# Performance work log

Hardware: AMD Instinct MI355X
Metric: run time of the kernel (lower is better)

## Reference

```python
import jax, jax.numpy as jnp
import numpy as np

B, N, D = 4, 2048, 512
OUT, H = 512, 8
HD = OUT // H

def setup_inputs() -> dict:
    key = jax.random.key(0)
    ks = jax.random.split(key, 10)
    s = 1.0 / np.sqrt(D)
    x = jax.random.normal(ks[0], (B, N, D), dtype=jnp.float32)
    adj = jax.random.randint(ks[1], (N, N), 0, 2, dtype=jnp.int32)
    Wq = jax.random.uniform(ks[2], (D, OUT), jnp.float32, -s, s)
    bq = jax.random.uniform(ks[3], (OUT,), jnp.float32, -s, s)
    Wk = jax.random.uniform(ks[4], (D, OUT), jnp.float32, -s, s)
    bk = jax.random.uniform(ks[5], (OUT,), jnp.float32, -s, s)
    Wv = jax.random.uniform(ks[6], (D, OUT), jnp.float32, -s, s)
    bv = jax.random.uniform(ks[7], (OUT,), jnp.float32, -s, s)
    so = 1.0 / np.sqrt(OUT)
    Wo = jax.random.uniform(ks[8], (OUT, OUT), jnp.float32, -so, so)
    bo = jax.random.uniform(ks[9], (OUT,), jnp.float32, -so, so)
    return {"x": x, "adj": adj, "Wq": Wq, "bq": bq, "Wk": Wk, "bk": bk,
            "Wv": Wv, "bv": bv, "Wo": Wo, "bo": bo}

def reference(x, adj, Wq, bq, Wk, bk, Wv, bv, Wo, bo):
    scale = HD ** -0.5
    # [B,N,OUT] -> [B,H,N,HD]
    def split_heads(t):
        return t.reshape(B, N, H, HD).transpose(0, 2, 1, 3)
    q = split_heads(x @ Wq + bq)
    k = split_heads(x @ Wk + bk)
    v = split_heads(x @ Wv + bv)
    attn = jnp.einsum('bhnd,bhmd->bhnm', q, k) * scale  # [B,H,N,N]
    mask = (adj == 0)[None, None, :, :]
    attn = jnp.where(mask, jnp.float32(-1e9), attn)
    attn = jax.nn.softmax(attn, axis=-1)
    out = jnp.einsum('bhnm,bhmd->bhnd', attn, v)
    out = out.transpose(0, 2, 1, 3).reshape(B, N, OUT)
    return out @ Wo + bo
```

## Files before the change

kernel.cpp:

```cpp
#include <hip/hip_runtime.h>
#include <math.h>

#define NB   4
#define NN   2048
#define DD   512
#define NOUT 512
#define NH   8
#define HDIM 64

typedef __attribute__((ext_vector_type(4))) short bf16x4;
typedef __attribute__((ext_vector_type(8))) short bf16x8;
typedef __attribute__((ext_vector_type(4))) float f32x4;
#define MFMA32(a, b, c)  __builtin_amdgcn_mfma_f32_16x16x32_bf16(a, b, c, 0, 0, 0)

typedef const __attribute__((address_space(1))) unsigned int* gas_ptr;
typedef __attribute__((address_space(3))) unsigned int* las_ptr;

#define SCALE2 0.18033688f


__device__ inline unsigned short f2bf(float f) {
    unsigned int u = __float_as_uint(f);
    u += 0x7fffu + ((u >> 16) & 1u);
    return (unsigned short)(u >> 16);
}

__device__ inline unsigned int pack_trunc(float lo, float hi) {
    return __builtin_amdgcn_perm(__float_as_uint(hi), __float_as_uint(lo), 0x07060302u);
}

__global__ __launch_bounds__(256) void prep(
    const float* __restrict__ x, unsigned short* __restrict__ xt,
    const float* __restrict__ W0, const float* __restrict__ W1,
    const float* __restrict__ W2, const float* __restrict__ W3,
    unsigned short* __restrict__ Tqkv, unsigned short* __restrict__ To,
    const int* __restrict__ adj, unsigned int* __restrict__ amaskW)
{
    const int blk = blockIdx.x;
    const int t   = threadIdx.x;

    if (blk < 2048) {
        const int i = (blk * 256 + t) * 8;
        const int m = i >> 9, k = i & 511;
        float4 a = *(const float4*)(x + i);
        float4 b = *(const float4*)(x + i + 4);
        ushort4 u0, u1;
        u0.x = f2bf(a.x); u0.y = f2bf(a.y); u0.z = f2bf(a.z); u0.w = f2bf(a.w);
        u1.x = f2bf(b.x); u1.y = f2bf(b.y); u1.z = f2bf(b.z); u1.w = f2bf(b.w);
        unsigned short* dst = xt + ((size_t)(m >> 7) * 65536)
                                 + (k >> 5) * 4096 + (m & 127) * 32 + (k & 31);
        *(ushort4*)dst       = u0;
        *(ushort4*)(dst + 4) = u1;
        return;
    }
    if (blk < 2304) {
        __shared__ float tile[64][65];
        const int idx = blk - 2048;
        const int z = idx >> 6, rem = idx & 63;
        const float* W;
        switch (z) {
            case 0:  W = W0; break;
            case 1:  W = W1; break;
            case 2:  W = W2; break;
            default: W = W3; break;
        }
        unsigned short* T = (z < 3) ? Tqkv : To;
        const int ngbase  = (z < 3) ? z * 512 : 0;
        const int k0 = (rem & 7) * 64, n0 = (rem >> 3) * 64;
        const int r = t >> 6, c = t & 63;
#pragma unroll
        for (int rep = 0; rep < 16; ++rep) {
            const int row = rep * 4 + r;
            tile[row][c] = W[(size_t)(k0 + row) * NOUT + n0 + c];
        }
        __syncthreads();
        const int k  = k0 + c;
        const int ks = k >> 5, kk = k & 31;
#pragma unroll
        for (int rep = 0; rep < 16; ++rep) {
            const int row = rep * 4 + r;
            const int ng  = ngbase + n0 + row;
            T[((size_t)(ng >> 7) * 65536) + ks * 4096 + (ng & 127) * 32 + kk]
                = f2bf(tile[c][row]);
        }
        return;
    }
    {
        const int gid  = (blk - 2304) * 256 + t;
        const int w0   = gid * 4;
        const int qrow = w0 >> 10;
        const int wloc = w0 & 1023;
        const int kb0  = wloc * 2;
        int4 a0 = *(const int4*)(adj + (size_t)qrow * NN + kb0);
        int4 a1 = *(const int4*)(adj + (size_t)qrow * NN + kb0 + 4);
        uint4 m;
        m.x = (a0.x ? 0xFFFFu : 0u) | (a0.y ? 0xFFFF0000u : 0u);
        m.y = (a0.z ? 0xFFFFu : 0u) | (a0.w ? 0xFFFF0000u : 0u);
        m.z = (a1.x ? 0xFFFFu : 0u) | (a1.y ? 0xFFFF0000u : 0u);
        m.w = (a1.z ? 0xFFFFu : 0u) | (a1.w ? 0xFFFF0000u : 0u);
        *(uint4*)(amaskW + (size_t)qrow * 1024 + wloc) = m;
    }
}

#define GT_SETUP(Atil, Wtil)                                                   \
    const int t = threadIdx.x, wave = t >> 6, lane = t & 63;                   \
    const int quad = lane >> 4, l16 = lane & 15;                               \
    const int n0 = blockIdx.x * 128, m0 = blockIdx.y * 128;                    \
    const int wm = (wave & 1) * 64, wn = (wave >> 1) * 64;                     \
    const unsigned short* aP[4];                                               \
    const unsigned short* bP[4];                                               \
    _Pragma("unroll")                                                          \
    for (int mt = 0; mt < 4; ++mt)                                             \
        aP[mt] = Atil + (size_t)blockIdx.y * 65536                             \
               + (wm + mt * 16 + l16) * 32 + quad * 8;                         \
    _Pragma("unroll")                                                          \
    for (int nt = 0; nt < 4; ++nt)                                             \
        bP[nt] = Wtil + (size_t)blockIdx.x * 65536                             \
               + (wn + nt * 16 + l16) * 32 + quad * 8;

#define GT_LOADF(Af, Bf, NTC, ks)                                              \
    _Pragma("unroll")                                                          \
    for (int mt = 0; mt < 4; ++mt) Af[mt] = *(const bf16x8*)(aP[mt] + (ks) * 4096); \
    _Pragma("unroll")                                                          \
    for (int nt = 0; nt < NTC; ++nt) Bf[nt] = *(const bf16x8*)(bP[nt] + (ks) * 4096);

#define GT_MFMA(Af, Bf, NTC)                                                   \
    _Pragma("unroll")                                                          \
    for (int mt = 0; mt < 4; ++mt)                                             \
        _Pragma("unroll")                                                      \
        for (int nt = 0; nt < NTC; ++nt)                                       \
            acc[mt][nt] = MFMA32(Af[mt], Bf[nt], acc[mt][nt]);

#define GT_LOOP(NTC)                                                           \
    f32x4 acc[4][NTC];                                                         \
    _Pragma("unroll")                                                          \
    for (int mt = 0; mt < 4; ++mt)                                             \
        _Pragma("unroll")                                                      \
        for (int nt = 0; nt < NTC; ++nt) acc[mt][nt] = (f32x4){0.f, 0.f, 0.f, 0.f}; \
    bf16x8 aA[4], bA[NTC], aB[4], bB[NTC];                                     \
    GT_LOADF(aA, bA, NTC, 0);                                                  \
    for (int kk = 0; kk < 8; ++kk) {                                           \
        GT_LOADF(aB, bB, NTC, 2 * kk + 1);                                     \
        GT_MFMA(aA, bA, NTC);                                                  \
        if (kk < 7) { GT_LOADF(aA, bA, NTC, 2 * kk + 2); }                     \
        GT_MFMA(aB, bB, NTC);                                                  \
    }

__global__ __launch_bounds__(256, 3) void gemm_qkv(
    const unsigned short* __restrict__ Atil,
    const unsigned short* __restrict__ Wtil,
    const float* __restrict__ bq, const float* __restrict__ bk,
    const float* __restrict__ bv,
    unsigned short* __restrict__ qo, unsigned short* __restrict__ ko,
    unsigned short* __restrict__ vto)
{
    __shared__ unsigned short eps[4 * 2560];
    GT_SETUP(Atil, Wtil);
    GT_LOOP(4);

    const int seg   = n0 >> 9;
    const int nloc0 = n0 & 511;
    const float* bp = (seg == 0) ? bq : (seg == 1) ? bk : bv;
    unsigned short* dst3 = (seg == 0) ? qo : (seg == 1) ? ko : vto;
    const int h = (nloc0 + wn) >> 6;

    float bias4[4];
#pragma unroll
    for (int nt = 0; nt < 4; ++nt) bias4[nt] = bp[nloc0 + wn + nt * 16 + l16];

    unsigned short* Lo = eps + wave * 2560;
#pragma unroll
    for (int mt = 0; mt < 4; ++mt) {
        if (seg < 2) {
#pragma unroll
            for (int nt = 0; nt < 4; ++nt)
#pragma unroll
                for (int r = 0; r < 4; ++r) {
                    float val = acc[mt][nt][r] + bias4[nt];
                    if (seg == 0) val *= SCALE2;
                    Lo[(quad * 4 + r) * 72 + nt * 16 + l16] = f2bf(val);
                }
#pragma unroll
            for (int pass = 0; pass < 2; ++pass) {
                const int row = pass * 8 + (lane >> 3);
                const int mg  = m0 + wm + mt * 16 + row;
                const int bb  = mg >> 11, n = mg & (NN - 1);
                bf16x8 v = *(const bf16x8*)&Lo[row * 72 + (lane & 7) * 8];
                *(bf16x8*)(dst3 + ((size_t)(bb * NH + h) * NN + n) * HDIM
                           + (lane & 7) * 8) = v;
            }
        } else {
#pragma unroll
            for (int nt = 0; nt < 4; ++nt)
#pragma unroll
                for (int r = 0; r < 4; ++r) {
                    const float val = acc[mt][nt][r] + bias4[nt];
                    Lo[(nt * 16 + l16) * 40 + quad * 4 + r] = f2bf(val);
                }
            const int d  = lane;
            const int mg = m0 + wm + mt * 16;
            const int bb = mg >> 11, n = mg & (NN - 1);
            unsigned short* dr = dst3 + ((size_t)(bb * NH + h) * HDIM + d) * NN + n;
            *(bf16x8*)dr       = *(const bf16x8*)&Lo[d * 40];
            *(bf16x8*)(dr + 8) = *(const bf16x8*)&Lo[d * 40 + 8];
        }
    }
}

__global__ __launch_bounds__(256, 3) void gemm_o(
    const unsigned short* __restrict__ Atil,
    const unsigned short* __restrict__ Wtil,
    const float* __restrict__ bias,
    float* __restrict__ C)
{
    const int t = threadIdx.x, wave = t >> 6, lane = t & 63;
    const int quad = lane >> 4, l16 = lane & 15;
    const int n0 = blockIdx.x * 64, m0 = blockIdx.y * 128;
    const int wm = (wave & 1) * 64, wn = (wave >> 1) * 32;
    const unsigned short* aP[4];
    const unsigned short* bP[2];
#pragma unroll
    for (int mt = 0; mt < 4; ++mt)
        aP[mt] = Atil + (size_t)blockIdx.y * 65536
               + (wm + mt * 16 + l16) * 32 + quad * 8;
#pragma unroll
    for (int nt = 0; nt < 2; ++nt)
        bP[nt] = Wtil + (size_t)(n0 >> 7) * 65536
               + ((n0 & 64) + wn + nt * 16 + l16) * 32 + quad * 8;

    GT_LOOP(2);

    float bias2[2];
#pragma unroll
    for (int nt = 0; nt < 2; ++nt) bias2[nt] = bias[n0 + wn + nt * 16 + l16];

#pragma unroll
    for (int mt = 0; mt < 4; ++mt)
#pragma unroll
        for (int nt = 0; nt < 2; ++nt) {
            const int col = n0 + wn + nt * 16 + l16;
#pragma unroll
            for (int r = 0; r < 4; ++r) {
                const int row = m0 + wm + mt * 16 + quad * 4 + r;
                C[(size_t)row * NOUT + col] = acc[mt][nt][r] + bias2[nt];
            }
        }
}

__global__ __launch_bounds__(512, 4) void attn_mfma(
    const unsigned short* __restrict__ qg,
    const unsigned short* __restrict__ kg,
    const unsigned short* __restrict__ vt,
    const unsigned int* __restrict__ amask,
    unsigned short* __restrict__ aot)
{
    __shared__ unsigned short smem[18432];
    unsigned short* Ka = smem;
    unsigned short* Va = smem + 4096;
    unsigned short* Kb = smem + 8192;
    unsigned short* Vb = smem + 12288;

    const int t    = threadIdx.x;
    const int wave = t >> 6;
    const int lane = t & 63;
    const int quad = lane >> 4;
    const int l16  = lane & 15;
    const int pair = wave >> 1;
    const int hk   = wave & 1;

    const int qt = blockIdx.x, h = blockIdx.y, b = blockIdx.z;
    const int bh = b * NH + h;
    const int q0 = qt * 128;

    const unsigned short* kbase  = kg + (size_t)bh * NN * HDIM;
    const unsigned short* vtbase = vt + (size_t)bh * HDIM * NN;

    const int drow = lane >> 3;
    const int dblk = (lane & 7) ^ drow;
    const int p  = wave * 8 + drow;
    const int Lp = (p & 32) + ((p >> 2) & 3) * 8 + ((p >> 4) & 1) * 4 + (p & 3);

    const int sw  = l16 & 7;
    const int bo0 = (quad ^ sw) * 8;
    const int bo1 = bo0 ^ 32;

#define ATT_ISSUE(kt, Kd, Vd)                                                  \
    {                                                                          \
        const int r0 = wave * 8;                                               \
        __builtin_amdgcn_global_load_lds(                                      \
            (gas_ptr)(kbase + (size_t)((kt) * 64 + Lp) * HDIM + dblk * 8),     \
            (las_ptr)(Kd + r0 * 64), 16, 0, 0);                                \
        __builtin_amdgcn_global_load_lds(                                      \
            (gas_ptr)(vtbase + (size_t)(r0 + drow) * NN + (kt) * 64 + dblk * 8), \
            (las_ptr)(Vd + r0 * 64), 16, 0, 0);                                \
    }

    const int myq0 = q0 + pair * 32 + l16;
    const int myq1 = myq0 + 16;
    const unsigned short* qrow0 = qg + ((size_t)bh * NN + myq0) * HDIM;
    const unsigned short* qrow1 = qg + ((size_t)bh * NN + myq1) * HDIM;
    const bf16x8 bQ0g0 = *(const bf16x8*)(qrow0 + quad * 8);
    const bf16x8 bQ1g0 = *(const bf16x8*)(qrow0 + quad * 8 + 32);
    const bf16x8 bQ0g1 = *(const bf16x8*)(qrow1 + quad * 8);
    const bf16x8 bQ1g1 = *(const bf16x8*)(qrow1 + quad * 8 + 32);

    const unsigned int* mrow0 = amask + (size_t)myq0 * 1024 + quad * 4;
    const unsigned int* mrow1 = amask + (size_t)myq1 * 1024 + quad * 4;
#define MLOAD(kt, g) (*(const uint4*)(((g) ? mrow1 : mrow0) + (kt) * 32 + hk * 16))

    bf16x8 ones8;
#pragma unroll
    for (int j = 0; j < 8; ++j) ones8[j] = (short)0x3F80;

    f32x4 O[4][2];
#pragma unroll
    for (int dt = 0; dt < 4; ++dt)
#pragma unroll
        for (int g = 0; g < 2; ++g) O[dt][g] = (f32x4){0.f, 0.f, 0.f, 0.f};
    f32x4 lacc[2];
    lacc[0] = (f32x4){0.f, 0.f, 0.f, 0.f};
    lacc[1] = (f32x4){0.f, 0.f, 0.f, 0.f};

    auto tile = [&](const unsigned short* Ks, const unsigned short* Vs,
                    uint4 mwg0, uint4 mwg1) {
        bf16x8 aK[2][2];
#pragma unroll
        for (int kg = 0; kg < 2; ++kg) {
            const int nt = hk * 2 + kg;
            aK[kg][0] = *(const bf16x8*)&Ks[(nt * 16 + l16) * 64 + bo0];
            aK[kg][1] = *(const bf16x8*)&Ks[(nt * 16 + l16) * 64 + bo1];
        }
        bf16x8 Pt[2];
#pragma unroll
        for (int g = 0; g < 2; ++g) {
            const uint4 mw = g ? mwg1 : mwg0;
            const bf16x8 q0f = g ? bQ0g1 : bQ0g0;
            const bf16x8 q1f = g ? bQ1g1 : bQ1g0;
            union { unsigned int u[4]; bf16x8 v; } cv;
#pragma unroll
            for (int kg = 0; kg < 2; ++kg) {
                f32x4 s = (f32x4){0.f, 0.f, 0.f, 0.f};
                s = MFMA32(aK[kg][0], q0f, s);
                s = MFMA32(aK[kg][1], q1f, s);
                const float p0 = exp2f(s[0]);
                const float p1 = exp2f(s[1]);
                const float p2 = exp2f(s[2]);
                const float p3 = exp2f(s[3]);
                cv.u[kg * 2 + 0] = pack_trunc(p0, p1) & (kg ? mw.z : mw.x);
                cv.u[kg * 2 + 1] = pack_trunc(p2, p3) & (kg ? mw.w : mw.y);
            }
            Pt[g] = cv.v;
            lacc[g] = MFMA32(ones8, Pt[g], lacc[g]);
        }
#pragma unroll
        for (int dt = 0; dt < 4; ++dt) {
            bf16x8 aV = *(const bf16x8*)
                &Vs[(dt * 16 + l16) * 64 + (((hk * 4 + quad) ^ sw) * 8)];
#pragma unroll
            for (int g = 0; g < 2; ++g)
                O[dt][g] = MFMA32(aV, Pt[g], O[dt][g]);
        }
    };

    uint4 mA0 = MLOAD(0, 0), mA1 = MLOAD(0, 1);
    uint4 mB0, mB1;
    ATT_ISSUE(0, Ka, Va);
    for (int kk = 0; kk < 16; ++kk) {
        __syncthreads();
        ATT_ISSUE(2 * kk + 1, Kb, Vb);
        mB0 = MLOAD(2 * kk + 1, 0); mB1 = MLOAD(2 * kk + 1, 1);
        tile(Ka, Va, mA0, mA1);
        __syncthreads();
        if (kk < 15) {
            ATT_ISSUE(2 * kk + 2, Ka, Va);
            mA0 = MLOAD(2 * kk + 2, 0); mA1 = MLOAD(2 * kk + 2, 1);
        }
        tile(Kb, Vb, mB0, mB1);
    }
    __syncthreads();

    float* F   = (float*)smem;
    float* myF = F + ((size_t)pair * 64 + lane) * 36;
    if (hk == 1) {
#pragma unroll
        for (int dt = 0; dt < 4; ++dt)
#pragma unroll
            for (int g = 0; g < 2; ++g)
                *(f32x4*)(myF + dt * 8 + g * 4) = O[dt][g];
        myF[32] = lacc[0][0];
        myF[33] = lacc[1][0];
    }
    __syncthreads();
    float inv0 = 0.f, inv1 = 0.f;
    if (hk == 0) {
#pragma unroll
        for (int dt = 0; dt < 4; ++dt)
#pragma unroll
            for (int g = 0; g < 2; ++g) {
                const f32x4 o2 = *(const f32x4*)(myF + dt * 8 + g * 4);
                O[dt][g] += o2;
            }
        inv0 = 1.f / (lacc[0][0] + myF[32]);
        inv1 = 1.f / (lacc[1][0] + myF[33]);
    }
    __syncthreads();

    if (hk == 0) {
#pragma unroll
        for (int g = 0; g < 2; ++g) {
            const float inv = g ? inv1 : inv0;
            unsigned short* Lo = smem + (pair * 2 + g) * 1152;
#pragma unroll
            for (int dt = 0; dt < 4; ++dt) {
                const float v0 = O[dt][g][0] * inv, v1 = O[dt][g][1] * inv;
                const float v2 = O[dt][g][2] * inv, v3 = O[dt][g][3] * inv;
                *(unsigned int*)&Lo[l16 * 72 + dt * 16 + quad * 4]     = pack_trunc(v0, v1);
                *(unsigned int*)&Lo[l16 * 72 + dt * 16 + quad * 4 + 2] = pack_trunc(v2, v3);
            }
            const int rr = lane >> 2;
            const int qq = q0 + pair * 32 + g * 16 + rr;
            const int m  = b * NN + qq;
            const int mb = m >> 7, r = m & 127;
#pragma unroll
            for (int i = 0; i < 2; ++i) {
                const int ch = (lane & 3) + 4 * i;
                const int ks = h * 2 + (ch >> 2);
                bf16x8 val = *(const bf16x8*)&Lo[rr * 72 + ch * 8];
                *(bf16x8*)(aot + (size_t)mb * 65536 + ks * 4096 + r * 32 + (ch & 3) * 8) = val;
            }
        }
    }
#undef ATT_ISSUE
#undef MLOAD
}

extern "C" void kernel_launch(void* const* d_in, const int* in_sizes, int n_in,
                              void* d_out, int out_size, void* d_ws, size_t ws_size,
                              hipStream_t stream)
{
    const float* x   = (const float*)d_in[0];
    const int*   adj = (const int*)  d_in[1];
    const float* Wq  = (const float*)d_in[2];
    const float* bq  = (const float*)d_in[3];
    const float* Wk  = (const float*)d_in[4];
    const float* bk  = (const float*)d_in[5];
    const float* Wv  = (const float*)d_in[6];
    const float* bv  = (const float*)d_in[7];
    const float* Wo  = (const float*)d_in[8];
    const float* bo  = (const float*)d_in[9];
    float* out = (float*)d_out;

    const size_t qkv_elems = (size_t)NB * NH * NN * HDIM;
    unsigned short* xt    = (unsigned short*)d_ws;
    unsigned short* q     = xt   + qkv_elems;
    unsigned short* kb    = q    + qkv_elems;
    unsigned short* vtb   = kb   + qkv_elems;
    unsigned short* tWqkv = vtb  + qkv_elems;
    unsigned short* tWo   = tWqkv + (size_t)3 * DD * NOUT;
    unsigned int*   amaskW = (unsigned int*)(tWo + (size_t)DD * NOUT);
    unsigned short* aot   = xt;

    prep<<<dim3(4352), 256, 0, stream>>>(x, xt, Wq, Wk, Wv, Wo,
                                         tWqkv, tWo, adj, amaskW);

    gemm_qkv<<<dim3(12, 64), 256, 0, stream>>>(xt, tWqkv, bq, bk, bv, q, kb, vtb);

    attn_mfma<<<dim3(NN / 128, NH, NB), 512, 0, stream>>>(q, kb, vtb, amaskW, aot);

    gemm_o<<<dim3(8, 64), 256, 0, stream>>>(aot, tWo, bo, out);
}
```

Measured before the change: 192.5 us.

## Triple-buffer K/V tiles with one barrier per tile and manual vmcnt waits

Replaces the double-buffered K/V loop, which used two __syncthreads per pair of tiles, with a three-slot ring buffer. Each iteration issues the load two tiles ahead and synchronises with an explicit s_waitcnt vmcnt plus a raw s_barrier. The goal is to hide more global-load latency and cut barrier count. Shared memory grows from 36KB to 48KB, which may lower occupancy at 4 blocks per CU. The hand-counted vmcnt values depend on how many loads ATT_ISSUE emits per tile, which makes correctness fragile.

```diff
diff --git a/kernel.cpp b/kernel.cpp
--- a/kernel.cpp
+++ b/kernel.cpp
@@ -254,11 +254,7 @@
     const unsigned int* __restrict__ amask,
     unsigned short* __restrict__ aot)
 {
-    __shared__ unsigned short smem[18432];
-    unsigned short* Ka = smem;
-    unsigned short* Va = smem + 4096;
-    unsigned short* Kb = smem + 8192;
-    unsigned short* Vb = smem + 12288;
+    __shared__ unsigned short smem[24576];
 
     const int t    = threadIdx.x;
     const int wave = t >> 6;
@@ -362,21 +358,30 @@
         }
     };
 
-    uint4 mA0 = MLOAD(0, 0), mA1 = MLOAD(0, 1);
-    uint4 mB0, mB1;
-    ATT_ISSUE(0, Ka, Va);
-    for (int kk = 0; kk < 16; ++kk) {
-        __syncthreads();
-        ATT_ISSUE(2 * kk + 1, Kb, Vb);
-        mB0 = MLOAD(2 * kk + 1, 0); mB1 = MLOAD(2 * kk + 1, 1);
-        tile(Ka, Va, mA0, mA1);
-        __syncthreads();
-        if (kk < 15) {
-            ATT_ISSUE(2 * kk + 2, Ka, Va);
-            mA0 = MLOAD(2 * kk + 2, 0); mA1 = MLOAD(2 * kk + 2, 1);
-        }
-        tile(Kb, Vb, mB0, mB1);
-    }
+    unsigned short* pK0 = smem;          unsigned short* pV0 = smem + 4096;
+    unsigned short* pK1 = smem + 8192;   unsigned short* pV1 = smem + 12288;
+    unsigned short* pK2 = smem + 16384;  unsigned short* pV2 = smem + 20480;
+
+    uint4 m0_ = MLOAD(0, 0), m1_ = MLOAD(0, 1);
+    asm volatile("" ::: "memory");
+    ATT_ISSUE(0, pK0, pV0);
+    asm volatile("" ::: "memory");
+    ATT_ISSUE(1, pK1, pV1);
+
+    for (int tt = 0; tt < 31; ++tt) {
+        if (tt == 0) asm volatile("s_waitcnt vmcnt(2)" ::: "memory");
+        else         asm volatile("s_waitcnt vmcnt(4)" ::: "memory");
+        __builtin_amdgcn_s_barrier();
+        uint4 n0_ = MLOAD(tt + 1, 0), n1_ = MLOAD(tt + 1, 1);
+        if (tt < 30) ATT_ISSUE(tt + 2, pK2, pV2);
+        tile(pK0, pV0, m0_, m1_);
+        m0_ = n0_; m1_ = n1_;
+        unsigned short* k0 = pK0; pK0 = pK1; pK1 = pK2; pK2 = k0;
+        unsigned short* v0 = pV0; pV0 = pV1; pV1 = pV2; pV2 = v0;
+    }
+    asm volatile("s_waitcnt vmcnt(0)" ::: "memory");
+    __builtin_amdgcn_s_barrier();
+    tile(pK0, pV0, m0_, m1_);
     __syncthreads();
 
     float* F   = (float*)smem;
```

Measured after the change: 197.3 us. 2.5% more time.

## Halve attention block to 4 waves, each handling 64 query rows

Applied to the files above, without the earlier changes.

The attention kernel now runs 256 threads per block instead of 512. Each wave pair covers 64 query rows (four 16-row groups) rather than 32, so every K fragment read from LDS feeds twice as many MFMAs, and each wave issues twice as many global-to-LDS loads. The change also swaps exp2f for the raw hardware exp2 builtin when it is available. In exchange, register pressure rises from the doubled O and lacc accumulators. Occupancy and latency hiding may also suffer, since launch bounds drop to 256 threads with 2 blocks per CU.

```diff
diff --git a/kernel.cpp b/kernel.cpp
--- a/kernel.cpp
+++ b/kernel.cpp
@@ -28,6 +28,12 @@
 __device__ inline unsigned int pack_trunc(float lo, float hi) {
     return __builtin_amdgcn_perm(__float_as_uint(hi), __float_as_uint(lo), 0x07060302u);
 }
+
+#if __has_builtin(__builtin_amdgcn_exp2f)
+#define EXP2(x) __builtin_amdgcn_exp2f(x)
+#else
+#define EXP2(x) exp2f(x)
+#endif
 
 __global__ __launch_bounds__(256) void prep(
     const float* __restrict__ x, unsigned short* __restrict__ xt,
@@ -247,7 +253,7 @@
         }
 }
 
-__global__ __launch_bounds__(512, 4) void attn_mfma(
+__global__ __launch_bounds__(256, 2) void attn_mfma(
     const unsigned short* __restrict__ qg,
     const unsigned short* __restrict__ kg,
     const unsigned short* __restrict__ vt,
@@ -277,8 +283,10 @@
 
     const int drow = lane >> 3;
     const int dblk = (lane & 7) ^ drow;
-    const int p  = wave * 8 + drow;
-    const int Lp = (p & 32) + ((p >> 2) & 3) * 8 + ((p >> 4) & 1) * 4 + (p & 3);
+    const int p0_ = wave * 16 + drow;
+    const int p1_ = p0_ + 8;
+    const int Lp0 = (p0_ & 32) + ((p0_ >> 2) & 3) * 8 + ((p0_ >> 4) & 1) * 4 + (p0_ & 3);
+    const int Lp1 = (p1_ & 32) + ((p1_ >> 2) & 3) * 8 + ((p1_ >> 4) & 1) * 4 + (p1_ & 3);
 
     const int sw  = l16 & 7;
     const int bo0 = (quad ^ sw) * 8;
@@ -286,43 +294,48 @@
 
 #define ATT_ISSUE(kt, Kd, Vd)                                                  \
     {                                                                          \
-        const int r0 = wave * 8;                                               \
+        const int r0 = wave * 16;                                              \
         __builtin_amdgcn_global_load_lds(                                      \
-            (gas_ptr)(kbase + (size_t)((kt) * 64 + Lp) * HDIM + dblk * 8),     \
+            (gas_ptr)(kbase + (size_t)((kt) * 64 + Lp0) * HDIM + dblk * 8),    \
             (las_ptr)(Kd + r0 * 64), 16, 0, 0);                                \
+        __builtin_amdgcn_global_load_lds(                                      \
+            (gas_ptr)(kbase + (size_t)((kt) * 64 + Lp1) * HDIM + dblk * 8),    \
+            (las_ptr)(Kd + (r0 + 8) * 64), 16, 0, 0);                          \
         __builtin_amdgcn_global_load_lds(                                      \
             (gas_ptr)(vtbase + (size_t)(r0 + drow) * NN + (kt) * 64 + dblk * 8), \
             (las_ptr)(Vd + r0 * 64), 16, 0, 0);                                \
-    }
-
-    const int myq0 = q0 + pair * 32 + l16;
-    const int myq1 = myq0 + 16;
-    const unsigned short* qrow0 = qg + ((size_t)bh * NN + myq0) * HDIM;
-    const unsigned short* qrow1 = qg + ((size_t)bh * NN + myq1) * HDIM;
-    const bf16x8 bQ0g0 = *(const bf16x8*)(qrow0 + quad * 8);
-    const bf16x8 bQ1g0 = *(const bf16x8*)(qrow0 + quad * 8 + 32);
-    const bf16x8 bQ0g1 = *(const bf16x8*)(qrow1 + quad * 8);
-    const bf16x8 bQ1g1 = *(const bf16x8*)(qrow1 + quad * 8 + 32);
-
-    const unsigned int* mrow0 = amask + (size_t)myq0 * 1024 + quad * 4;
-    const unsigned int* mrow1 = amask + (size_t)myq1 * 1024 + quad * 4;
-#define MLOAD(kt, g) (*(const uint4*)(((g) ? mrow1 : mrow0) + (kt) * 32 + hk * 16))
+        __builtin_amdgcn_global_load_lds(                                      \
+            (gas_ptr)(vtbase + (size_t)(r0 + 8 + drow) * NN + (kt) * 64 + dblk * 8), \
+            (las_ptr)(Vd + (r0 + 8) * 64), 16, 0, 0);                          \
+    }
+
+    bf16x8 bQ0[4], bQ1[4];
+    const unsigned int* mrow[4];
+#pragma unroll
+    for (int g = 0; g < 4; ++g) {
+        const int myq = q0 + pair * 64 + g * 16 + l16;
+        const unsigned short* qr = qg + ((size_t)bh * NN + myq) * HDIM;
+        bQ0[g] = *(const bf16x8*)(qr + quad * 8);
+        bQ1[g] = *(const bf16x8*)(qr + quad * 8 + 32);
+        mrow[g] = amask + (size_t)myq * 1024 + quad * 4;
+    }
+#define MLOAD(kt, g) (*(const uint4*)(mrow[g] + (kt) * 32 + hk * 16))
 
     bf16x8 ones8;
 #pragma unroll
     for (int j = 0; j < 8; ++j) ones8[j] = (short)0x3F80;
 
-    f32x4 O[4][2];
+    f32x4 O[4][4];
 #pragma unroll
     for (int dt = 0; dt < 4; ++dt)
 #pragma unroll
-        for (int g = 0; g < 2; ++g) O[dt][g] = (f32x4){0.f, 0.f, 0.f, 0.f};
-    f32x4 lacc[2];
-    lacc[0] = (f32x4){0.f, 0.f, 0.f, 0.f};
-    lacc[1] = (f32x4){0.f, 0.f, 0.f, 0.f};
+        for (int g = 0; g < 4; ++g) O[dt][g] = (f32x4){0.f, 0.f, 0.f, 0.f};
+    f32x4 lacc[4];
+#pragma unroll
+    for (int g = 0; g < 4; ++g) lacc[g] = (f32x4){0.f, 0.f, 0.f, 0.f};
 
     auto tile = [&](const unsigned short* Ks, const unsigned short* Vs,
-                    uint4 mwg0, uint4 mwg1) {
+                    uint4 w0, uint4 w1, uint4 w2, uint4 w3) {
         bf16x8 aK[2][2];
 #pragma unroll
         for (int kg = 0; kg < 2; ++kg) {
@@ -330,22 +343,20 @@
             aK[kg][0] = *(const bf16x8*)&Ks[(nt * 16 + l16) * 64 + bo0];
             aK[kg][1] = *(const bf16x8*)&Ks[(nt * 16 + l16) * 64 + bo1];
         }
-        bf16x8 Pt[2];
-#pragma unroll
-        for (int g = 0; g < 2; ++g) {
-            const uint4 mw = g ? mwg1 : mwg0;
-            const bf16x8 q0f = g ? bQ0g1 : bQ0g0;
-            const bf16x8 q1f = g ? bQ1g1 : bQ1g0;
+        bf16x8 Pt[4];
+#pragma unroll
+        for (int g = 0; g < 4; ++g) {
+            const uint4 mw = (g == 0) ? w0 : (g == 1) ? w1 : (g == 2) ? w2 : w3;
             union { unsigned int u[4]; bf16x8 v; } cv;
 #pragma unroll
             for (int kg = 0; kg < 2; ++kg) {
                 f32x4 s = (f32x4){0.f, 0.f, 0.f, 0.f};
-                s = MFMA32(aK[kg][0], q0f, s);
-                s = MFMA32(aK[kg][1], q1f, s);
-                const float p0 = exp2f(s[0]);
-                const float p1 = exp2f(s[1]);
-                const float p2 = exp2f(s[2]);
-                const float p3 = exp2f(s[3]);
+                s = MFMA32(aK[kg][0], bQ0[g], s);
+                s = MFMA32(aK[kg][1], bQ1[g], s);
+                const float p0 = EXP2(s[0]);
+                const float p1 = EXP2(s[1]);
+                const float p2 = EXP2(s[2]);
+                const float p3 = EXP2(s[3]);
                 cv.u[kg * 2 + 0] = pack_trunc(p0, p1) & (kg ? mw.z : mw.x);
                 cv.u[kg * 2 + 1] = pack_trunc(p2, p3) & (kg ? mw.w : mw.y);
             }
@@ -357,68 +368,70 @@
             bf16x8 aV = *(const bf16x8*)
                 &Vs[(dt * 16 + l16) * 64 + (((hk * 4 + quad) ^ sw) * 8)];
 #pragma unroll
-            for (int g = 0; g < 2; ++g)
+            for (int g = 0; g < 4; ++g)
                 O[dt][g] = MFMA32(aV, Pt[g], O[dt][g]);
         }
     };
 
-    uint4 mA0 = MLOAD(0, 0), mA1 = MLOAD(0, 1);
-    uint4 mB0, mB1;
+    uint4 mA0 = MLOAD(0, 0), mA1 = MLOAD(0, 1), mA2 = MLOAD(0, 2), mA3 = MLOAD(0, 3);
+    uint4 mB0, mB1, mB2, mB3;
     ATT_ISSUE(0, Ka, Va);
     for (int kk = 0; kk < 16; ++kk) {
         __syncthreads();
         ATT_ISSUE(2 * kk + 1, Kb, Vb);
         mB0 = MLOAD(2 * kk + 1, 0); mB1 = MLOAD(2 * kk + 1, 1);
-        tile(Ka, Va, mA0, mA1);
+        mB2 = MLOAD(2 * kk + 1, 2); mB3 = MLOAD(2 * kk + 1, 3);
+        tile(Ka, Va, mA0, mA1, mA2, mA3);
         __syncthreads();
         if (kk < 15) {
             ATT_ISSUE(2 * kk + 2, Ka, Va);
             mA0 = MLOAD(2 * kk + 2, 0); mA1 = MLOAD(2 * kk + 2, 1);
-        }
-        tile(Kb, Vb, mB0, mB1);
+            mA2 = MLOAD(2 * kk + 2, 2); mA3 = MLOAD(2 * kk + 2, 3);
+        }
+        tile(Kb, Vb, mB0, mB1, mB2, mB3);
     }
     __syncthreads();
 
     float* F   = (float*)smem;
-    float* myF = F + ((size_t)pair * 64 + lane) * 36;
+    float* myF = F + ((size_t)(pair * 64 + lane)) * 68;
     if (hk == 1) {
 #pragma unroll
         for (int dt = 0; dt < 4; ++dt)
 #pragma unroll
-            for (int g = 0; g < 2; ++g)
-                *(f32x4*)(myF + dt * 8 + g * 4) = O[dt][g];
-        myF[32] = lacc[0][0];
-        myF[33] = lacc[1][0];
+            for (int g = 0; g < 4; ++g)
+                *(f32x4*)(myF + dt * 16 + g * 4) = O[dt][g];
+#pragma unroll
+        for (int g = 0; g < 4; ++g) myF[64 + g] = lacc[g][0];
     }
     __syncthreads();
-    float inv0 = 0.f, inv1 = 0.f;
+    float inv[4] = {0.f, 0.f, 0.f, 0.f};
     if (hk == 0) {
 #pragma unroll
         for (int dt = 0; dt < 4; ++dt)
 #pragma unroll
-            for (int g = 0; g < 2; ++g) {
-                const f32x4 o2 = *(const f32x4*)(myF + dt * 8 + g * 4);
+            for (int g = 0; g < 4; ++g) {
+                const f32x4 o2 = *(const f32x4*)(myF + dt * 16 + g * 4);
                 O[dt][g] += o2;
             }
-        inv0 = 1.f / (lacc[0][0] + myF[32]);
-        inv1 = 1.f / (lacc[1][0] + myF[33]);
+#pragma unroll
+        for (int g = 0; g < 4; ++g)
+            inv[g] = 1.f / (lacc[g][0] + myF[64 + g]);
     }
     __syncthreads();
 
     if (hk == 0) {
 #pragma unroll
-        for (int g = 0; g < 2; ++g) {
-            const float inv = g ? inv1 : inv0;
-            unsigned short* Lo = smem + (pair * 2 + g) * 1152;
+        for (int g = 0; g < 4; ++g) {
+            unsigned short* Lo = smem + (pair * 4 + g) * 1152;
 #pragma unroll
             for (int dt = 0; dt < 4; ++dt) {
-                const float v0 = O[dt][g][0] * inv, v1 = O[dt][g][1] * inv;
-                const float v2 = O[dt][g][2] * inv, v3 = O[dt][g][3] * inv;
+                const float v0 = O[dt][g][0] * inv[g], v1 = O[dt][g][1] * inv[g];
+                const float v2 = O[dt][g][2] * inv[g], v3 = O[dt][g][3] * inv[g];
                 *(unsigned int*)&Lo[l16 * 72 + dt * 16 + quad * 4]     = pack_trunc(v0, v1);
                 *(unsigned int*)&Lo[l16 * 72 + dt * 16 + quad * 4 + 2] = pack_trunc(v2, v3);
             }
             const int rr = lane >> 2;
-            const int qq = q0 + pair * 32 + g * 16 + rr;
+            const int qq = q0 + pair * 64 + g * 16 + rr;
             const int m  = b * NN + qq;
             const int mb = m >> 7, r = m & 127;
 #pragma unroll
@@ -465,7 +478,7 @@
 
     gemm_qkv<<<dim3(12, 64), 256, 0, stream>>>(xt, tWqkv, bq, bk, bv, q, kb, vtb);
 
-    attn_mfma<<<dim3(NN / 128, NH, NB), 512, 0, stream>>>(q, kb, vtb, amaskW, aot);
+    attn_mfma<<<dim3(NN / 128, NH, NB), 256, 0, stream>>>(q, kb, vtb, amaskW, aot);
 
     gemm_o<<<dim3(8, 64), 256, 0, stream>>>(aot, tWo, bo, out);
 }
```

Measured after the change: 189.2 us. Within noise of the previous version (-1.8%).
